# Performance work log

Measured on AMD Instinct MI355X. Metric: run time of the kernel, lower is better.

The kernel has to match this reference:

```python
import jax, jax.numpy as jnp
import numpy as np

N_HEAD = 12

def fillnan(x):
    return jnp.nan_to_num(x, nan=0.0, posinf=0.0, neginf=0.0)

def setup_inputs() -> dict:
    key = jax.random.key(0)
    k1, k2, k3 = jax.random.split(key, 3)
    B, T, C = 2, 2048, 768
    x = jax.random.normal(k1, (B, T, C), dtype=jnp.float32)
    W_attn = jax.random.normal(k2, (3 * C, C), dtype=jnp.float32) * 0.02
    W_proj = jax.random.normal(k3, (C, C), dtype=jnp.float32) * 0.02
    return {"x": x, "W_attn": W_attn, "W_proj": W_proj}

def reference(x, W_attn, W_proj):
    B, T, C = x.shape
    H = N_HEAD
    D = C // H
    # qkv projection (torch Linear: x @ W^T), then nan-sanitize
    qkv = fillnan(jnp.einsum('btc,fc->btf', x, W_attn))  # [B,T,3C]
    q, k, v = jnp.split(qkv, 3, axis=-1)
    # [B,T,C] -> [B,H,T,D]
    q = q.reshape(B, T, H, D).transpose(0, 2, 1, 3)
    k = k.reshape(B, T, H, D).transpose(0, 2, 1, 3)
    v = v.reshape(B, T, H, D).transpose(0, 2, 1, 3)
    scale = 1.0 / np.sqrt(D).astype(np.float32)
    att = jnp.einsum('bhqd,bhkd->bhqk', q, k) * scale  # [B,H,T,T]
    att = fillnan(att)
    causal = jnp.tril(jnp.ones((T, T), dtype=bool))
    att = jnp.where(causal[None, None], att, -jnp.inf)
    att = jax.nn.softmax(att, axis=-1)
    att = fillnan(att)
    y = jnp.einsum('bhqk,bhkd->bhqd', att, v)  # [B,H,T,D]
    y = fillnan(y)
    y = y.transpose(0, 2, 1, 3).reshape(B, T, C)
    y = fillnan(jnp.einsum('btc,fc->btf', y, W_proj))
    return y
```

## Files before the change

kernel.cpp:

```cpp
#include <hip/hip_runtime.h>

typedef __attribute__((ext_vector_type(8))) short bf16x8;
typedef __attribute__((ext_vector_type(4))) float f32x4;

__device__ __forceinline__ unsigned short f2b(float f) {
  union { float f; unsigned u; } v; v.f = f;
  return (unsigned short)((v.u + 0x7FFFu + ((v.u >> 16) & 1u)) >> 16);
}
__device__ __forceinline__ unsigned short f2b_fast(float f) {
  union { float f; unsigned u; } v; v.f = f;
  return (unsigned short)((v.u + 0x8000u) >> 16);
}

#define XN4   786432
#define WAN4  442368
#define WPN4  147456
__global__ void cvt_all(const float* __restrict__ x, const float* __restrict__ Wa,
                        const float* __restrict__ Wp,
                        unsigned short* __restrict__ xb, unsigned short* __restrict__ Wab,
                        unsigned short* __restrict__ Wpb) {
  int i = blockIdx.x * 256 + threadIdx.x;
  const float* src; unsigned short* dst; int off;
  if (i < XN4)            { src = x;  dst = xb;  off = i; }
  else if (i < XN4 + WAN4){ src = Wa; dst = Wab; off = i - XN4; }
  else                    { src = Wp; dst = Wpb; off = i - XN4 - WAN4; }
  float4 f = reinterpret_cast<const float4*>(src)[off];
  ushort4 o;
  o.x = f2b(f.x); o.y = f2b(f.y); o.z = f2b(f.z); o.w = f2b(f.w);
  reinterpret_cast<ushort4*>(dst)[off] = o;
}

#define BM 128
#define BN 128
#define BK 64

__global__ __launch_bounds__(256, 2)
void gemm_nt(const unsigned short* __restrict__ A,
             const unsigned short* __restrict__ Bm,
             int M, int N, int K, int mode,
             unsigned short* __restrict__ qb,
             unsigned short* __restrict__ kb_,
             unsigned short* __restrict__ vt,
             float* __restrict__ outf) {
  __shared__ unsigned short As[BM * BK];
  __shared__ unsigned short Bs[BN * BK];
  int tid = threadIdx.x;
  int wave = tid >> 6, lane = tid & 63;
  int quad = lane >> 4, l16 = lane & 15;
  int m0 = blockIdx.x * BM, n0 = blockIdx.y * BN;
  int wm = (wave & 1) * 64, wn = (wave >> 1) * 64;

  int srow = lane >> 3;
  int scol = ((lane & 7) ^ srow) << 3;

  f32x4 acc[4][4] = {};

  for (int k0 = 0; k0 < K; k0 += BK) {
    __syncthreads();
#pragma unroll
    for (int i = 0; i < 4; ++i) {
      int r = wave * 32 + i * 8;
      __builtin_amdgcn_global_load_lds(
          (const __attribute__((address_space(1))) unsigned int*)(A + (size_t)(m0 + r + srow) * K + k0 + scol),
          (__attribute__((address_space(3))) unsigned int*)(As + r * BK), 16, 0, 0);
      __builtin_amdgcn_global_load_lds(
          (const __attribute__((address_space(1))) unsigned int*)(Bm + (size_t)(n0 + r + srow) * K + k0 + scol),
          (__attribute__((address_space(3))) unsigned int*)(Bs + r * BK), 16, 0, 0);
    }
    __syncthreads();
#pragma unroll
    for (int kb = 0; kb < 2; ++kb) {
      int ch = (((kb << 2) | quad) ^ (l16 & 7)) << 3;
      bf16x8 af[4], bf[4];
#pragma unroll
      for (int i = 0; i < 4; ++i)
        af[i] = *reinterpret_cast<const bf16x8*>(As + (wm + i * 16 + l16) * BK + ch);
#pragma unroll
      for (int j = 0; j < 4; ++j)
        bf[j] = *reinterpret_cast<const bf16x8*>(Bs + (wn + j * 16 + l16) * BK + ch);
#pragma unroll
      for (int i = 0; i < 4; ++i)
#pragma unroll
        for (int j = 0; j < 4; ++j)
          acc[i][j] = __builtin_amdgcn_mfma_f32_16x16x32_bf16(af[i], bf[j], acc[i][j], 0, 0, 0);
    }
  }

  const float scale2 = 0.125f * 1.44269504089f;
#pragma unroll
  for (int i = 0; i < 4; ++i) {
    int mbase = m0 + wm + i * 16 + quad * 4;
#pragma unroll
    for (int j = 0; j < 4; ++j) {
      int f = n0 + wn + j * 16 + l16;
#pragma unroll
      for (int r = 0; r < 4; ++r) {
        float c = acc[i][j][r];
        int m = mbase + r;
        if (mode == 0) {
          int b = m >> 11, t = m & 2047;
          int which = f / 768;
          int f2 = f - which * 768;
          int h = f2 >> 6, d = f2 & 63;
          int bh = b * 12 + h;
          if (which == 0)      qb[((size_t)(bh * 2048 + t)) * 64 + d] = f2b(c * scale2);
          else if (which == 1) kb_[((size_t)(bh * 2048 + t)) * 64 + d] = f2b(c);
          else                 vt[((size_t)(bh * 64 + d)) * 2048 + t] = f2b(c);
        } else {
          outf[(size_t)m * N + f] = c;
        }
      }
    }
  }
}

#define PLDP 72

__global__ __launch_bounds__(256, 3)
void attn_part(const unsigned short* __restrict__ Qb,
               const unsigned short* __restrict__ Kb,
               const unsigned short* __restrict__ Vt,
               float* __restrict__ Opart, float* __restrict__ Lpart) {
  __shared__ unsigned short Ks[2][64 * 64];
  __shared__ unsigned short Vs[2][64 * 64];
  __shared__ unsigned short P[4 * 32 * PLDP];
  const int T = 2048, D = 64;
  int wave = threadIdx.x >> 6, lane = threadIdx.x & 63;
  int quad = lane >> 4, l16 = lane & 15;

  int w = blockIdx.x;
  int bh = w / 40;
  int r = 39 - (w - bh * 40);
  int qb, ci;
  if (r < 4)       { qb = r;                 ci = 0; }
  else if (r < 12) { qb = 4 + ((r - 4) >> 1);  ci = (r - 4) & 1; }
  else if (r < 24) { qb = 8 + (r - 12) / 3;    ci = (r - 12) % 3; }
  else             { qb = 12 + ((r - 24) >> 2); ci = (r - 24) & 3; }
  int nk = 2 * qb + 2;
  int nc = (qb >> 2) + 1;
  int t0 = ci * nk / nc, t1 = (ci + 1) * nk / nc;

  int q0 = qb * 128;
  int qrow = q0 + wave * 32;

  const unsigned short* Qp = Qb + (size_t)bh * T * D;
  const unsigned short* Kp = Kb + (size_t)bh * T * D;
  const unsigned short* Vp = Vt + (size_t)bh * D * T;
  unsigned short* Pw = P + wave * 32 * PLDP;

  int srow = lane >> 3;
  int scol = ((lane & 7) ^ srow) << 3;

  bf16x8 aq[2][2];
#pragma unroll
  for (int qi = 0; qi < 2; ++qi)
#pragma unroll
    for (int cc = 0; cc < 2; ++cc)
      aq[qi][cc] = *reinterpret_cast<const bf16x8*>(
          Qp + (qrow + qi * 16 + l16) * D + cc * 32 + quad * 8);

  bf16x8 ones;
#pragma unroll
  for (int e = 0; e < 8; ++e) ones[e] = (short)0x3F80;

  f32x4 o[2][4] = {};
  f32x4 lacc[2] = {};

#define STAGE_KV(buf, k0s)                                                          \
  {                                                                                 \
    _Pragma("unroll")                                                               \
    for (int i_ = 0; i_ < 2; ++i_) {                                                \
      int rr_ = wave * 16 + i_ * 8;                                                 \
      __builtin_amdgcn_global_load_lds(                                             \
          (const __attribute__((address_space(1))) unsigned int*)(Kp + (size_t)((k0s) + rr_ + srow) * 64 + scol), \
          (__attribute__((address_space(3))) unsigned int*)(&Ks[buf][rr_ * 64]), 16, 0, 0); \
      __builtin_amdgcn_global_load_lds(                                             \
          (const __attribute__((address_space(1))) unsigned int*)(Vp + (size_t)(rr_ + srow) * 2048 + (k0s) + scol), \
          (__attribute__((address_space(3))) unsigned int*)(&Vs[buf][rr_ * 64]), 16, 0, 0); \
    }                                                                               \
  }

  STAGE_KV(0, t0 << 6);
  asm volatile("s_waitcnt vmcnt(0)" ::: "memory");
  __builtin_amdgcn_s_barrier();

  int cur = 0;
  for (int t = t0; t < t1; ++t) {
    int k0 = t << 6;
    if (t + 1 < t1) STAGE_KV(cur ^ 1, (t + 1) << 6);

    if (k0 <= qrow + 31) {
      f32x4 sacc[2][4] = {};
      __builtin_amdgcn_s_setprio(1);
#pragma unroll
      for (int nt2 = 0; nt2 < 4; ++nt2) {
        bf16x8 bk0 = *reinterpret_cast<const bf16x8*>(Ks[cur] + (nt2 * 16 + l16) * 64 + ((quad ^ (l16 & 7)) << 3));
        bf16x8 bk1 = *reinterpret_cast<const bf16x8*>(Ks[cur] + (nt2 * 16 + l16) * 64 + (((4 | quad) ^ (l16 & 7)) << 3));
#pragma unroll
        for (int qi = 0; qi < 2; ++qi) {
          sacc[qi][nt2] = __builtin_amdgcn_mfma_f32_16x16x32_bf16(aq[qi][0], bk0, sacc[qi][nt2], 0, 0, 0);
          sacc[qi][nt2] = __builtin_amdgcn_mfma_f32_16x16x32_bf16(aq[qi][1], bk1, sacc[qi][nt2], 0, 0, 0);
        }
      }
      __builtin_amdgcn_s_setprio(0);

      if (k0 + 63 > qrow) {
#pragma unroll
        for (int qi = 0; qi < 2; ++qi)
#pragma unroll
          for (int nt2 = 0; nt2 < 4; ++nt2) {
            int col = k0 + nt2 * 16 + l16;
#pragma unroll
            for (int rr = 0; rr < 4; ++rr) {
              int row = qrow + qi * 16 + quad * 4 + rr;
              sacc[qi][nt2][rr] = (col <= row) ? sacc[qi][nt2][rr] : -1e30f;
            }
          }
      }
#pragma unroll
      for (int qi = 0; qi < 2; ++qi)
#pragma unroll
        for (int nt2 = 0; nt2 < 4; ++nt2)
#pragma unroll
          for (int rr = 0; rr < 4; ++rr)
            sacc[qi][nt2][rr] = exp2f(sacc[qi][nt2][rr]);

#pragma unroll
      for (int qi = 0; qi < 2; ++qi)
#pragma unroll
        for (int nt2 = 0; nt2 < 4; ++nt2)
#pragma unroll
          for (int rr = 0; rr < 4; ++rr)
            Pw[(qi * 16 + quad * 4 + rr) * PLDP + nt2 * 16 + l16] = f2b_fast(sacc[qi][nt2][rr]);
      __asm__ volatile("s_waitcnt lgkmcnt(0)" ::: "memory");

      bf16x8 vf[4][2];
#pragma unroll
      for (int dt = 0; dt < 4; ++dt) {
        vf[dt][0] = *reinterpret_cast<const bf16x8*>(Vs[cur] + (dt * 16 + l16) * 64 + ((quad ^ (l16 & 7)) << 3));
        vf[dt][1] = *reinterpret_cast<const bf16x8*>(Vs[cur] + (dt * 16 + l16) * 64 + (((4 | quad) ^ (l16 & 7)) << 3));
      }
      __builtin_amdgcn_s_setprio(1);
#pragma unroll
      for (int qi = 0; qi < 2; ++qi) {
        bf16x8 ap0 = *reinterpret_cast<const bf16x8*>(Pw + (qi * 16 + l16) * PLDP + quad * 8);
        bf16x8 ap1 = *reinterpret_cast<const bf16x8*>(Pw + (qi * 16 + l16) * PLDP + 32 + quad * 8);
#pragma unroll
        for (int dt = 0; dt < 4; ++dt) {
          o[qi][dt] = __builtin_amdgcn_mfma_f32_16x16x32_bf16(ap0, vf[dt][0], o[qi][dt], 0, 0, 0);
          o[qi][dt] = __builtin_amdgcn_mfma_f32_16x16x32_bf16(ap1, vf[dt][1], o[qi][dt], 0, 0, 0);
        }
        lacc[qi] = __builtin_amdgcn_mfma_f32_16x16x32_bf16(ap0, ones, lacc[qi], 0, 0, 0);
        lacc[qi] = __builtin_amdgcn_mfma_f32_16x16x32_bf16(ap1, ones, lacc[qi], 0, 0, 0);
      }
      __builtin_amdgcn_s_setprio(0);
    }

    asm volatile("s_waitcnt vmcnt(0)" ::: "memory");
    __builtin_amdgcn_s_barrier();
    cur ^= 1;
  }

  float* Op = Opart + (size_t)blockIdx.x * 8192 + wave * 32 * 64;
#pragma unroll
  for (int qi = 0; qi < 2; ++qi)
#pragma unroll
    for (int dt = 0; dt < 4; ++dt)
#pragma unroll
      for (int rr = 0; rr < 4; ++rr)
        Op[(qi * 16 + quad * 4 + rr) * 64 + dt * 16 + l16] = o[qi][dt][rr];
  if (l16 == 0) {
#pragma unroll
    for (int qi = 0; qi < 2; ++qi)
#pragma unroll
      for (int rr = 0; rr < 4; ++rr)
        Lpart[blockIdx.x * 128 + wave * 32 + qi * 16 + quad * 4 + rr] = lacc[qi][rr];
  }
}

__global__ __launch_bounds__(256)
void attn_combine(const float* __restrict__ Opart, const float* __restrict__ Lpart,
                  unsigned short* __restrict__ Yb) {
  int blk = blockIdx.x;
  int bh = blk >> 4, qb = blk & 15;
  int off = (qb < 4) ? qb : (qb < 8) ? 4 + 2 * (qb - 4)
          : (qb < 12) ? 12 + 3 * (qb - 8) : 24 + 4 * (qb - 12);
  int nc = (qb >> 2) + 1;
  int b = bh / 12, h = bh - b * 12;
  int q0 = qb * 128;
#pragma unroll
  for (int i = 0; i < 8; ++i) {
    int idx = i * 256 + threadIdx.x;
    int row = idx >> 4, c4 = idx & 15;
    float4 s = {0.f, 0.f, 0.f, 0.f};
    float L = 0.f;
    for (int ci = 0; ci < nc; ++ci) {
      size_t pb = (size_t)(bh * 40 + 39 - (off + ci));
      float4 v = *reinterpret_cast<const float4*>(Opart + pb * 8192 + row * 64 + c4 * 4);
      s.x += v.x; s.y += v.y; s.z += v.z; s.w += v.w;
      L += Lpart[pb * 128 + row];
    }
    float rl = 1.0f / L;
    ushort4 y;
    y.x = f2b(s.x * rl); y.y = f2b(s.y * rl);
    y.z = f2b(s.z * rl); y.w = f2b(s.w * rl);
    *reinterpret_cast<ushort4*>(Yb + ((size_t)(b * 2048 + q0 + row)) * 768 + h * 64 + c4 * 4) = y;
  }
}

extern "C" void kernel_launch(void* const* d_in, const int* in_sizes, int n_in,
                              void* d_out, int out_size, void* d_ws, size_t ws_size,
                              hipStream_t stream) {
  const float* x  = (const float*)d_in[0];
  const float* Wa = (const float*)d_in[1];
  const float* Wp = (const float*)d_in[2];
  float* out = (float*)d_out;

  unsigned short* ws = (unsigned short*)d_ws;
  unsigned short* xb  = ws;
  unsigned short* Wab = xb  + 3145728;
  unsigned short* Wpb = Wab + 1769472;
  unsigned short* Qb  = Wpb + 589824;
  unsigned short* Kb  = Qb  + 3145728;
  unsigned short* Vt  = Kb  + 3145728;
  unsigned short* Yb  = Vt  + 3145728;
  float*          Opart = (float*)(Yb + 3145728);
  float*          Lpart = Opart + 7864320;

  cvt_all<<<(XN4 + WAN4 + WPN4) / 256, 256, 0, stream>>>(x, Wa, Wp, xb, Wab, Wpb);

  gemm_nt<<<dim3(4096 / BM, 2304 / BN), 256, 0, stream>>>(
      xb, Wab, 4096, 2304, 768, 0, Qb, Kb, Vt, nullptr);

  attn_part<<<960, 256, 0, stream>>>(Qb, Kb, Vt, Opart, Lpart);
  attn_combine<<<384, 256, 0, stream>>>(Opart, Lpart, Yb);

  gemm_nt<<<dim3(4096 / BM, 768 / BN), 256, 0, stream>>>(
      Yb, Wpb, 4096, 768, 768, 1, nullptr, nullptr, nullptr, out);
}
```

Baseline: 163.6 us.

## Compute transposed scores and shuffle P via bpermute instead of LDS round-trip

Swaps the MFMA operand order so each lane holds scores for one query across consecutive keys, then packs P to bf16 with v_cvt_pk_bf16_f32 and rearranges it into the A-operand layout with ds_bpermute. This removes the per-wave shared-memory P buffer and its store/wait/load round-trip, and raises launch bounds from 3 to 4 blocks per CU now that LDS use is smaller. The cost is extra bpermute and select instructions plus tighter register limits from the higher occupancy target; the rounding also changes from the fast add-0x8000 conversion to the hardware conversion.

```diff
diff --git a/kernel.cpp b/kernel.cpp
--- a/kernel.cpp
+++ b/kernel.cpp
@@ -6,10 +6,6 @@
 __device__ __forceinline__ unsigned short f2b(float f) {
   union { float f; unsigned u; } v; v.f = f;
   return (unsigned short)((v.u + 0x7FFFu + ((v.u >> 16) & 1u)) >> 16);
-}
-__device__ __forceinline__ unsigned short f2b_fast(float f) {
-  union { float f; unsigned u; } v; v.f = f;
-  return (unsigned short)((v.u + 0x8000u) >> 16);
 }
 
 #define XN4   786432
@@ -114,18 +110,16 @@
   }
 }
 
-#define PLDP 72
-
-__global__ __launch_bounds__(256, 3)
+__global__ __launch_bounds__(256, 4)
 void attn_part(const unsigned short* __restrict__ Qb,
                const unsigned short* __restrict__ Kb,
                const unsigned short* __restrict__ Vt,
                float* __restrict__ Opart, float* __restrict__ Lpart) {
   __shared__ unsigned short Ks[2][64 * 64];
   __shared__ unsigned short Vs[2][64 * 64];
-  __shared__ unsigned short P[4 * 32 * PLDP];
   const int T = 2048, D = 64;
-  int wave = threadIdx.x >> 6, lane = threadIdx.x & 63;
+  int lane = threadIdx.x & 63;
+  int wave = threadIdx.x >> 6;
   int quad = lane >> 4, l16 = lane & 15;
 
   int w = blockIdx.x;
@@ -146,7 +140,6 @@
   const unsigned short* Qp = Qb + (size_t)bh * T * D;
   const unsigned short* Kp = Kb + (size_t)bh * T * D;
   const unsigned short* Vp = Vt + (size_t)bh * D * T;
-  unsigned short* Pw = P + wave * 32 * PLDP;
 
   int srow = lane >> 3;
   int scol = ((lane & 7) ^ srow) << 3;
@@ -165,6 +158,10 @@
 
   f32x4 o[2][4] = {};
   f32x4 lacc[2] = {};
+
+  int hi = (lane >> 5) & 1;
+  int adr0 = (((lane >> 4) & 1) * 32 + l16) << 2;
+  int adr1 = adr0 + (16 << 2);
 
 #define STAGE_KV(buf, k0s)                                                          \
   {                                                                                 \
@@ -190,49 +187,40 @@
     if (t + 1 < t1) STAGE_KV(cur ^ 1, (t + 1) << 6);
 
     if (k0 <= qrow + 31) {
-      f32x4 sacc[2][4] = {};
+      f32x4 st[4][2] = {};
       __builtin_amdgcn_s_setprio(1);
 #pragma unroll
-      for (int nt2 = 0; nt2 < 4; ++nt2) {
-        bf16x8 bk0 = *reinterpret_cast<const bf16x8*>(Ks[cur] + (nt2 * 16 + l16) * 64 + ((quad ^ (l16 & 7)) << 3));
-        bf16x8 bk1 = *reinterpret_cast<const bf16x8*>(Ks[cur] + (nt2 * 16 + l16) * 64 + (((4 | quad) ^ (l16 & 7)) << 3));
+      for (int kt = 0; kt < 4; ++kt) {
+        bf16x8 ak0 = *reinterpret_cast<const bf16x8*>(Ks[cur] + (kt * 16 + l16) * 64 + ((quad ^ (l16 & 7)) << 3));
+        bf16x8 ak1 = *reinterpret_cast<const bf16x8*>(Ks[cur] + (kt * 16 + l16) * 64 + (((4 | quad) ^ (l16 & 7)) << 3));
 #pragma unroll
         for (int qi = 0; qi < 2; ++qi) {
-          sacc[qi][nt2] = __builtin_amdgcn_mfma_f32_16x16x32_bf16(aq[qi][0], bk0, sacc[qi][nt2], 0, 0, 0);
-          sacc[qi][nt2] = __builtin_amdgcn_mfma_f32_16x16x32_bf16(aq[qi][1], bk1, sacc[qi][nt2], 0, 0, 0);
+          st[kt][qi] = __builtin_amdgcn_mfma_f32_16x16x32_bf16(ak0, aq[qi][0], st[kt][qi], 0, 0, 0);
+          st[kt][qi] = __builtin_amdgcn_mfma_f32_16x16x32_bf16(ak1, aq[qi][1], st[kt][qi], 0, 0, 0);
         }
       }
       __builtin_amdgcn_s_setprio(0);
 
       if (k0 + 63 > qrow) {
 #pragma unroll
-        for (int qi = 0; qi < 2; ++qi)
-#pragma unroll
-          for (int nt2 = 0; nt2 < 4; ++nt2) {
-            int col = k0 + nt2 * 16 + l16;
+        for (int kt = 0; kt < 4; ++kt)
+#pragma unroll
+          for (int qi = 0; qi < 2; ++qi) {
+            int q = qrow + qi * 16 + l16;
 #pragma unroll
             for (int rr = 0; rr < 4; ++rr) {
-              int row = qrow + qi * 16 + quad * 4 + rr;
-              sacc[qi][nt2][rr] = (col <= row) ? sacc[qi][nt2][rr] : -1e30f;
+              int key = k0 + kt * 16 + quad * 4 + rr;
+              st[kt][qi][rr] = (key <= q) ? st[kt][qi][rr] : -1e30f;
             }
           }
       }
 #pragma unroll
-      for (int qi = 0; qi < 2; ++qi)
-#pragma unroll
-        for (int nt2 = 0; nt2 < 4; ++nt2)
+      for (int kt = 0; kt < 4; ++kt)
+#pragma unroll
+        for (int qi = 0; qi < 2; ++qi)
 #pragma unroll
           for (int rr = 0; rr < 4; ++rr)
-            sacc[qi][nt2][rr] = exp2f(sacc[qi][nt2][rr]);
-
-#pragma unroll
-      for (int qi = 0; qi < 2; ++qi)
-#pragma unroll
-        for (int nt2 = 0; nt2 < 4; ++nt2)
-#pragma unroll
-          for (int rr = 0; rr < 4; ++rr)
-            Pw[(qi * 16 + quad * 4 + rr) * PLDP + nt2 * 16 + l16] = f2b_fast(sacc[qi][nt2][rr]);
-      __asm__ volatile("s_waitcnt lgkmcnt(0)" ::: "memory");
+            st[kt][qi][rr] = __builtin_amdgcn_exp2f(st[kt][qi][rr]);
 
       bf16x8 vf[4][2];
 #pragma unroll
@@ -240,18 +228,46 @@
         vf[dt][0] = *reinterpret_cast<const bf16x8*>(Vs[cur] + (dt * 16 + l16) * 64 + ((quad ^ (l16 & 7)) << 3));
         vf[dt][1] = *reinterpret_cast<const bf16x8*>(Vs[cur] + (dt * 16 + l16) * 64 + (((4 | quad) ^ (l16 & 7)) << 3));
       }
+
+      bf16x8 pa[2][2];
+#pragma unroll
+      for (int qi = 0; qi < 2; ++qi) {
+        int pk[4][2];
+#pragma unroll
+        for (int kt = 0; kt < 4; ++kt)
+#pragma unroll
+          for (int h = 0; h < 2; ++h)
+            asm("v_cvt_pk_bf16_f32 %0, %1, %2"
+                : "=v"(pk[kt][h])
+                : "v"(st[kt][qi][2 * h]), "v"(st[kt][qi][2 * h + 1]));
+#pragma unroll
+        for (int g = 0; g < 2; ++g) {
+          int wv[4];
+#pragma unroll
+          for (int w1 = 0; w1 < 2; ++w1)
+#pragma unroll
+            for (int w0 = 0; w0 < 2; ++w0) {
+              int a_ = w1 ? adr1 : adr0;
+              int r0_ = __builtin_amdgcn_ds_bpermute(a_, pk[2 * g + 0][w0]);
+              int r1_ = __builtin_amdgcn_ds_bpermute(a_, pk[2 * g + 1][w0]);
+              wv[w1 * 2 + w0] = hi ? r1_ : r0_;
+            }
+          union { int i[4]; bf16x8 v; } u_;
+          u_.i[0] = wv[0]; u_.i[1] = wv[1]; u_.i[2] = wv[2]; u_.i[3] = wv[3];
+          pa[qi][g] = u_.v;
+        }
+      }
+
       __builtin_amdgcn_s_setprio(1);
 #pragma unroll
       for (int qi = 0; qi < 2; ++qi) {
-        bf16x8 ap0 = *reinterpret_cast<const bf16x8*>(Pw + (qi * 16 + l16) * PLDP + quad * 8);
-        bf16x8 ap1 = *reinterpret_cast<const bf16x8*>(Pw + (qi * 16 + l16) * PLDP + 32 + quad * 8);
 #pragma unroll
         for (int dt = 0; dt < 4; ++dt) {
-          o[qi][dt] = __builtin_amdgcn_mfma_f32_16x16x32_bf16(ap0, vf[dt][0], o[qi][dt], 0, 0, 0);
-          o[qi][dt] = __builtin_amdgcn_mfma_f32_16x16x32_bf16(ap1, vf[dt][1], o[qi][dt], 0, 0, 0);
+          o[qi][dt] = __builtin_amdgcn_mfma_f32_16x16x32_bf16(pa[qi][0], vf[dt][0], o[qi][dt], 0, 0, 0);
+          o[qi][dt] = __builtin_amdgcn_mfma_f32_16x16x32_bf16(pa[qi][1], vf[dt][1], o[qi][dt], 0, 0, 0);
         }
-        lacc[qi] = __builtin_amdgcn_mfma_f32_16x16x32_bf16(ap0, ones, lacc[qi], 0, 0, 0);
-        lacc[qi] = __builtin_amdgcn_mfma_f32_16x16x32_bf16(ap1, ones, lacc[qi], 0, 0, 0);
+        lacc[qi] = __builtin_amdgcn_mfma_f32_16x16x32_bf16(pa[qi][0], ones, lacc[qi], 0, 0, 0);
+        lacc[qi] = __builtin_amdgcn_mfma_f32_16x16x32_bf16(pa[qi][1], ones, lacc[qi], 0, 0, 0);
       }
       __builtin_amdgcn_s_setprio(0);
     }
```

New measurement: 169.1 us. 1.03x slower.
